# Kernel optimization log

Measured on AMD Instinct MI355X. Metric: run time of the kernel, lower is better.

Reference implementation:

```python
import jax, jax.numpy as jnp
import numpy as np

B, W, H = 8, 1024, 1024
NUM_LABELS = 100  # mask ids in [0, NUM_LABELS); 0 = background
EPS = 1e-7


def setup_inputs() -> dict:
    key = jax.random.key(0)
    k1, k2 = jax.random.split(key)
    pred = jax.random.normal(k1, (B, 2, W, H), dtype=jnp.float32)
    mask = jax.random.randint(k2, (B, W, H), 0, NUM_LABELS, dtype=jnp.int32)
    ignored_map = jnp.ones((B, W, H), dtype=jnp.float32)
    return {"pred": pred, "mask": mask, "ignored_map": ignored_map}


def _smooth_l1(d):
    # SmoothL1Loss(reduction='none'), beta=1
    a = jnp.abs(d)
    return jnp.where(a < 1.0, 0.5 * d * d, a - 0.5)


def _gt_single(mask2d):
    # Vectorized replacement of the per-instance python loop:
    # segment-mean for centroids, segment-max for the per-instance `norm`.
    seg = mask2d.reshape(-1)  # [W*H]
    x_map = jnp.tile(jnp.arange(H, dtype=jnp.float32), W)    # column index (x)
    y_map = jnp.repeat(jnp.arange(W, dtype=jnp.float32), H)  # row index (y)
    cnt = jax.ops.segment_sum(jnp.ones_like(x_map), seg, num_segments=NUM_LABELS)
    safe_cnt = jnp.maximum(cnt, 1.0)
    xc = (jax.ops.segment_sum(x_map, seg, num_segments=NUM_LABELS) / safe_cnt)[seg]
    yc = (jax.ops.segment_sum(y_map, seg, num_segments=NUM_LABELS) / safe_cnt)[seg]
    fg = (seg != 0).astype(jnp.float32)  # label 0 is background (index_list[1:])
    vx = (x_map - xc) * fg  # (x_map - mean_x) * nuclei, instances are disjoint
    vy = (y_map - yc) * fg
    # torch.max over the whole image of (coord - c)*nuclei == max(seg_max, 0)
    mx = jnp.maximum(jax.ops.segment_max(vx, seg, num_segments=NUM_LABELS), 0.0)
    my = jnp.maximum(jax.ops.segment_max(vy, seg, num_segments=NUM_LABELS), 0.0)
    gx = vx / jnp.where(mx == 0.0, 1.0, mx)[seg]  # norm(): divide by max iff max != 0
    gy = vy / jnp.where(my == 0.0, 1.0, my)[seg]
    return jnp.stack([gx, gy]).reshape(2, W, H)


def reference(pred, mask, ignored_map):
    gt = jax.vmap(_gt_single)(mask)  # [B, 2, W, H]
    fg = (mask != 0).astype(jnp.float32)[:, None]  # [B, 1, W, H]
    bg = 1.0 - fg
    n = float(mask.size)
    # ((mask != 0) + 1e-07).sum() == fg_count + eps * numel
    fg_den = jnp.sum(fg) + EPS * n
    bg_den = jnp.sum(bg) + EPS * n
    d = _smooth_l1(pred - gt)
    ig = ignored_map[:, None]
    offset_loss = jnp.sum(d * ig * (fg / fg_den + bg / bg_den))
    return offset_loss, gt
```

## Files before the change

kernel.cpp:

```cpp
#include <hip/hip_runtime.h>

#define NL 100
#define BB 8
#define HH 1024
#define NPIX (1024 * 1024)
#define EPSF 1e-7f
#define NBLK 128
#define LBK 64
#define NLOSS (LBK * BB)

typedef float f4 __attribute__((ext_vector_type(4)));

#define OFF_ACC  0
#define OFF_TKT  1
#define OFF_M8   8
#define OFF_PART (OFF_M8 + BB * (NPIX / 4))
#define WS_NEED  ((size_t)(OFF_PART + 5 * BB * NL * NBLK) * 4)

__device__ __forceinline__ int pidx(int v, int b, int l) {
    return ((v * BB + b) * NL + l) * NBLK;
}

__global__ __launch_bounds__(256) void k_stats(const int* __restrict__ mask,
                                               unsigned* __restrict__ wsu) {
    __shared__ unsigned s_cs[4][2][NL];
    __shared__ unsigned s_mx[4][NL];
    __shared__ unsigned g_cnt[NL], g_sx[NL], g_sy[NL], g_mx[NL], g_my[NL];
    unsigned* part = wsu + OFF_PART;
    unsigned* m8   = wsu + OFF_M8;
    const int b    = blockIdx.y;
    const int blk  = blockIdx.x;
    const int wv   = threadIdx.x >> 6;
    const int lane = threadIdx.x & 63;
    if (blk == 0 && b == 0 && threadIdx.x == 0) {
        ((float*)wsu)[OFF_ACC] = 0.0f;
        wsu[OFF_TKT] = 0u;
    }
    for (int i = threadIdx.x; i < NL; i += 256) {
        g_cnt[i] = 0u; g_sx[i] = 0u; g_sy[i] = 0u; g_mx[i] = 0u; g_my[i] = 0u;
    }
    for (int i = lane; i < 2 * NL; i += 64) s_cs[wv][0][i] = 0u;
    for (int i = lane; i < NL; i += 64) s_mx[wv][i] = 0u;
    __syncthreads();

    const int4* m4  = (const int4*)(mask + (size_t)b * NPIX);
    unsigned*   m8b = m8 + (size_t)b * (NPIX / 4);
    const int y0 = blk * 8 + wv * 2;

    int4 R[2][4];
#pragma unroll
    for (int r = 0; r < 2; ++r)
#pragma unroll
        for (int it = 0; it < 4; ++it)
            R[r][it] = m4[(y0 + r) * 256 + it * 64 + lane];

#pragma unroll
    for (int r = 0; r < 2; ++r) {
        unsigned* tp = &s_cs[wv][r][0];
        unsigned* mp = &s_mx[wv][0];
        const int y = y0 + r;
#pragma unroll
        for (int it = 0; it < 4; ++it) {
            const int4 mv = R[r][it];
            const int c4 = it * 64 + lane;
            const unsigned v0 = (1u << 21) + (unsigned)(c4 << 2);
            atomicAdd(tp + mv.x, v0);      atomicMax(mp + mv.x, v0);
            atomicAdd(tp + mv.y, v0 + 1u); atomicMax(mp + mv.y, v0 + 1u);
            atomicAdd(tp + mv.z, v0 + 2u); atomicMax(mp + mv.z, v0 + 2u);
            atomicAdd(tp + mv.w, v0 + 3u); atomicMax(mp + mv.w, v0 + 3u);
            m8b[y * 256 + c4] = (unsigned)mv.x | ((unsigned)mv.y << 8) |
                                ((unsigned)mv.z << 16) | ((unsigned)mv.w << 24);
        }
    }
    for (int e = lane; e < NL; e += 64) {
        const unsigned cs0 = s_cs[wv][0][e];
        const unsigned cs1 = s_cs[wv][1][e];
        const unsigned c0 = cs0 >> 21, c1 = cs1 >> 21;
        const unsigned cnt = c0 + c1;
        if (cnt) {
            atomicAdd(&g_cnt[e], cnt);
            atomicAdd(&g_sx[e], (cs0 & 0x1FFFFFu) + (cs1 & 0x1FFFFFu));
            atomicAdd(&g_sy[e], c0 * (unsigned)y0 + c1 * (unsigned)(y0 + 1));
            atomicMax(&g_my[e], c1 ? (unsigned)(y0 + 1) : (unsigned)y0);
            atomicMax(&g_mx[e], s_mx[wv][e] & 0x1FFFFFu);
        }
    }
    __syncthreads();
    for (int e = threadIdx.x; e < NL; e += 256) {
        part[pidx(0, b, e) + blk] = g_cnt[e];
        part[pidx(1, b, e) + blk] = g_sx[e];
        part[pidx(2, b, e) + blk] = g_sy[e];
        part[pidx(3, b, e) + blk] = g_mx[e];
        part[pidx(4, b, e) + blk] = g_my[e];
    }
}

__global__ __launch_bounds__(256, 2) void k_loss(const float* __restrict__ pred,
                                                 const float* __restrict__ ig,
                                                 unsigned* __restrict__ wsu,
                                                 float* __restrict__ out) {
    __shared__ unsigned s_st[5][NL];
    __shared__ unsigned s_c0[BB];
    __shared__ f4 s_tab[NL];
    __shared__ float s_red[4];
    const unsigned* part = wsu + OFF_PART;
    const unsigned* m8   = wsu + OFF_M8;
    const int b   = blockIdx.y;
    const int tid = threadIdx.x;

    if (tid < BB) s_c0[tid] = 0u;
    __syncthreads();
    {
        const int bb = tid >> 5, j = tid & 31;
        const uint4* p4 = (const uint4*)(part + pidx(0, bb, 0));
        const uint4 u = p4[j];
        atomicAdd(&s_c0[bb], u.x + u.y + u.z + u.w);
    }
    for (int t = tid; t < 5 * NL; t += 256) {
        const int v = t / NL;
        const int l = t - v * NL;
        const uint4* p4 = (const uint4*)(part + pidx(v, b, l));
        unsigned s = 0u, m = 0u;
#pragma unroll 8
        for (int k = 0; k < NBLK / 4; ++k) {
            const uint4 u = p4[k];
            s += u.x + u.y + u.z + u.w;
            m = max(max(m, u.x), max(u.y, max(u.z, u.w)));
        }
        s_st[v][l] = (v >= 3) ? m : s;
    }
    __syncthreads();
    if (tid < NL) {
        const unsigned cnt = s_st[0][tid];
        const float sc = (float)(cnt ? cnt : 1u);
        const float xc = (float)s_st[1][tid] / sc;
        const float yc = (float)s_st[2][tid] / sc;
        float fmx = (float)s_st[3][tid] - xc; if (fmx < 0.0f) fmx = 0.0f;
        float fmy = (float)s_st[4][tid] - yc; if (fmy < 0.0f) fmy = 0.0f;
        f4 e;
        e.x = xc;
        e.y = yc;
        e.z = (fmx == 0.0f) ? 1.0f : 1.0f / fmx;
        e.w = (fmy == 0.0f) ? 1.0f : 1.0f / fmy;
        s_tab[tid] = e;
    }
    __syncthreads();
    float bgc = 0.0f;
#pragma unroll
    for (int i = 0; i < BB; ++i) bgc += (float)s_c0[i];
    const float n = (float)BB * (float)NPIX;
    const float inv_bg = 1.0f / (bgc + EPSF * n);
    const float inv_fg = 1.0f / ((n - bgc) + EPSF * n);

    const unsigned* m8b = m8 + (size_t)b * (NPIX / 4);
    const f4* ig4 = (const f4*)(ig + (size_t)b * NPIX);
    const f4* px4 = (const f4*)(pred + (size_t)(2 * b) * NPIX);
    const f4* py4 = (const f4*)(pred + (size_t)(2 * b + 1) * NPIX);
    f4* gx4 = (f4*)(out + 1 + (size_t)(2 * b) * NPIX);
    f4* gy4 = (f4*)(out + 1 + (size_t)(2 * b + 1) * NPIX);

    float acc = 0.0f;
#pragma unroll
    for (int g = 0; g < 4; ++g) {
        const int base = (blockIdx.x * 4 + g) * 1024;
        unsigned M8[4]; f4 IV[4], PX[4], PY[4];
#pragma unroll
        for (int it = 0; it < 4; ++it) {
            const int i4 = base + it * 256 + tid;
            M8[it] = m8b[i4];
            IV[it] = __builtin_nontemporal_load(&ig4[i4]);
            PX[it] = __builtin_nontemporal_load(&px4[i4]);
            PY[it] = __builtin_nontemporal_load(&py4[i4]);
        }
#pragma unroll
        for (int it = 0; it < 4; ++it) {
            const int i4 = base + it * 256 + tid;
            const int p  = i4 << 2;
            const float x0 = (float)(p & (HH - 1));
            const float y  = (float)(p >> 10);
            const float* igs = (const float*)&IV[it];
            const float* pxs = (const float*)&PX[it];
            const float* pys = (const float*)&PY[it];
            f4 gxv, gyv;
            float* gxa = (float*)&gxv;
            float* gya = (float*)&gyv;
#pragma unroll
            for (int j = 0; j < 4; ++j) {
                const int m = (int)((M8[it] >> (8 * j)) & 255u);
                const f4 t = s_tab[m];
                const float fgf = (m != 0) ? 1.0f : 0.0f;
                const float gx = (x0 + (float)j - t.x) * t.z * fgf;
                const float gy = (y - t.y) * t.w * fgf;
                const float w  = ((m != 0) ? inv_fg : inv_bg) * igs[j];
                const float dx = pxs[j] - gx;
                const float dy = pys[j] - gy;
                const float ax = fabsf(dx), ay = fabsf(dy);
                acc += ((ax < 1.0f) ? 0.5f * dx * dx : ax - 0.5f) * w
                     + ((ay < 1.0f) ? 0.5f * dy * dy : ay - 0.5f) * w;
                gxa[j] = gx;
                gya[j] = gy;
            }
            __builtin_nontemporal_store(gxv, &gx4[i4]);
            __builtin_nontemporal_store(gyv, &gy4[i4]);
        }
    }
#pragma unroll
    for (int off = 32; off > 0; off >>= 1) acc += __shfl_down(acc, off, 64);
    const int lane = tid & 63, wv = tid >> 6;
    if (lane == 0) s_red[wv] = acc;
    __syncthreads();
    if (tid == 0) {
        const float s = s_red[0] + s_red[1] + s_red[2] + s_red[3];
        atomicAdd((float*)wsu + OFF_ACC, s);
        __threadfence();
        const unsigned old = atomicAdd(wsu + OFF_TKT, 1u);
        if (old == NLOSS - 1) {
            __threadfence();
            out[0] = atomicAdd((float*)wsu + OFF_ACC, 0.0f);
        }
    }
}

extern "C" void kernel_launch(void* const* d_in, const int* in_sizes, int n_in,
                              void* d_out, int out_size, void* d_ws, size_t ws_size,
                              hipStream_t stream) {
    const float* pred = (const float*)d_in[0];
    const int*   mask = (const int*)d_in[1];
    const float* ig   = (const float*)d_in[2];
    float* out = (float*)d_out;
    unsigned* wsu = (unsigned*)d_ws;

    k_stats<<<dim3(NBLK, BB), 256, 0, stream>>>(mask, wsu);
    k_loss<<<dim3(LBK, BB), 256, 0, stream>>>(pred, ig, wsu, out);
}
```

Measured before the change: 211.5 us.

## Finalize per-label stats in last stats block; shrink loss blocks for occupancy

The per-image centroid/norm table is now built once by the last-arriving k_stats block, selected with a per-image ticket counter. Each k_loss block used to re-reduce all partials itself; now it just loads the finished table. The partial layout is transposed, and the loss grid grows to 256 blocks per image with one 1024-vector chunk each and launch bounds of 4, to raise parallelism and occupancy. A memset resets the counters before the launches, which adds a small extra operation per call.

```diff
diff --git a/kernel.cpp b/kernel.cpp
--- a/kernel.cpp
+++ b/kernel.cpp
@@ -6,19 +6,21 @@
 #define NPIX (1024 * 1024)
 #define EPSF 1e-7f
 #define NBLK 128
-#define LBK 64
-#define NLOSS (LBK * BB)
+#define LGX 256
+#define NLOSS (LGX * BB)
 
 typedef float f4 __attribute__((ext_vector_type(4)));
 
 #define OFF_ACC  0
 #define OFF_TKT  1
-#define OFF_M8   8
+#define OFF_STK  2
+#define OFF_TAB  16
+#define OFF_CNT0 (OFF_TAB + 4 * BB * NL)
+#define OFF_M8   (OFF_CNT0 + BB)
 #define OFF_PART (OFF_M8 + BB * (NPIX / 4))
-#define WS_NEED  ((size_t)(OFF_PART + 5 * BB * NL * NBLK) * 4)
-
-__device__ __forceinline__ int pidx(int v, int b, int l) {
-    return ((v * BB + b) * NL + l) * NBLK;
+
+__device__ __forceinline__ int part_idx(int v, int blk, int b, int l) {
+    return ((v * NBLK + blk) * BB + b) * NL + l;
 }
 
 __global__ __launch_bounds__(256) void k_stats(const int* __restrict__ mask,
@@ -26,16 +28,13 @@
     __shared__ unsigned s_cs[4][2][NL];
     __shared__ unsigned s_mx[4][NL];
     __shared__ unsigned g_cnt[NL], g_sx[NL], g_sy[NL], g_mx[NL], g_my[NL];
+    __shared__ int s_last;
     unsigned* part = wsu + OFF_PART;
     unsigned* m8   = wsu + OFF_M8;
     const int b    = blockIdx.y;
     const int blk  = blockIdx.x;
     const int wv   = threadIdx.x >> 6;
     const int lane = threadIdx.x & 63;
-    if (blk == 0 && b == 0 && threadIdx.x == 0) {
-        ((float*)wsu)[OFF_ACC] = 0.0f;
-        wsu[OFF_TKT] = 0u;
-    }
     for (int i = threadIdx.x; i < NL; i += 256) {
         g_cnt[i] = 0u; g_sx[i] = 0u; g_sy[i] = 0u; g_mx[i] = 0u; g_my[i] = 0u;
     }
@@ -87,63 +86,59 @@
     }
     __syncthreads();
     for (int e = threadIdx.x; e < NL; e += 256) {
-        part[pidx(0, b, e) + blk] = g_cnt[e];
-        part[pidx(1, b, e) + blk] = g_sx[e];
-        part[pidx(2, b, e) + blk] = g_sy[e];
-        part[pidx(3, b, e) + blk] = g_mx[e];
-        part[pidx(4, b, e) + blk] = g_my[e];
-    }
-}
-
-__global__ __launch_bounds__(256, 2) void k_loss(const float* __restrict__ pred,
-                                                 const float* __restrict__ ig,
-                                                 unsigned* __restrict__ wsu,
-                                                 float* __restrict__ out) {
-    __shared__ unsigned s_st[5][NL];
-    __shared__ unsigned s_c0[BB];
-    __shared__ f4 s_tab[NL];
-    __shared__ float s_red[4];
-    const unsigned* part = wsu + OFF_PART;
-    const unsigned* m8   = wsu + OFF_M8;
-    const int b   = blockIdx.y;
-    const int tid = threadIdx.x;
-
-    if (tid < BB) s_c0[tid] = 0u;
-    __syncthreads();
-    {
-        const int bb = tid >> 5, j = tid & 31;
-        const uint4* p4 = (const uint4*)(part + pidx(0, bb, 0));
-        const uint4 u = p4[j];
-        atomicAdd(&s_c0[bb], u.x + u.y + u.z + u.w);
-    }
-    for (int t = tid; t < 5 * NL; t += 256) {
-        const int v = t / NL;
-        const int l = t - v * NL;
-        const uint4* p4 = (const uint4*)(part + pidx(v, b, l));
-        unsigned s = 0u, m = 0u;
-#pragma unroll 8
-        for (int k = 0; k < NBLK / 4; ++k) {
-            const uint4 u = p4[k];
-            s += u.x + u.y + u.z + u.w;
-            m = max(max(m, u.x), max(u.y, max(u.z, u.w)));
-        }
-        s_st[v][l] = (v >= 3) ? m : s;
-    }
-    __syncthreads();
-    if (tid < NL) {
-        const unsigned cnt = s_st[0][tid];
+        part[part_idx(0, blk, b, e)] = g_cnt[e];
+        part[part_idx(1, blk, b, e)] = g_sx[e];
+        part[part_idx(2, blk, b, e)] = g_sy[e];
+        part[part_idx(3, blk, b, e)] = g_mx[e];
+        part[part_idx(4, blk, b, e)] = g_my[e];
+    }
+    __syncthreads();
+    if (threadIdx.x == 0) {
+        __threadfence();
+        const unsigned old = atomicAdd(wsu + OFF_STK + b, 1u);
+        s_last = (old == NBLK - 1) ? 1 : 0;
+    }
+    __syncthreads();
+    if (!s_last) return;
+    __threadfence();
+    if (threadIdx.x < NL) {
+        const int l = threadIdx.x;
+        unsigned cnt = 0, sx = 0, sy = 0, mx = 0, my = 0;
+#pragma unroll 4
+        for (int k = 0; k < NBLK; ++k) {
+            cnt += part[part_idx(0, k, b, l)];
+            sx  += part[part_idx(1, k, b, l)];
+            sy  += part[part_idx(2, k, b, l)];
+            mx = max(mx, part[part_idx(3, k, b, l)]);
+            my = max(my, part[part_idx(4, k, b, l)]);
+        }
         const float sc = (float)(cnt ? cnt : 1u);
-        const float xc = (float)s_st[1][tid] / sc;
-        const float yc = (float)s_st[2][tid] / sc;
-        float fmx = (float)s_st[3][tid] - xc; if (fmx < 0.0f) fmx = 0.0f;
-        float fmy = (float)s_st[4][tid] - yc; if (fmy < 0.0f) fmy = 0.0f;
+        const float xc = (float)sx / sc;
+        const float yc = (float)sy / sc;
+        float fmx = (float)mx - xc; if (fmx < 0.0f) fmx = 0.0f;
+        float fmy = (float)my - yc; if (fmy < 0.0f) fmy = 0.0f;
         f4 e;
         e.x = xc;
         e.y = yc;
         e.z = (fmx == 0.0f) ? 1.0f : 1.0f / fmx;
         e.w = (fmy == 0.0f) ? 1.0f : 1.0f / fmy;
-        s_tab[tid] = e;
-    }
+        ((f4*)(wsu + OFF_TAB))[b * NL + l] = e;
+        if (l == 0) wsu[OFF_CNT0 + b] = cnt;
+    }
+}
+
+__global__ __launch_bounds__(256, 4) void k_loss(const float* __restrict__ pred,
+                                                 const float* __restrict__ ig,
+                                                 unsigned* __restrict__ wsu,
+                                                 float* __restrict__ out) {
+    __shared__ f4 s_tab[NL];
+    __shared__ unsigned s_c0[BB];
+    __shared__ float s_part[4];
+    const unsigned* m8 = wsu + OFF_M8;
+    const int b = blockIdx.y;
+    for (int i = threadIdx.x; i < NL; i += 256)
+        s_tab[i] = ((const f4*)(wsu + OFF_TAB))[b * NL + i];
+    if (threadIdx.x < BB) s_c0[threadIdx.x] = wsu[OFF_CNT0 + threadIdx.x];
     __syncthreads();
     float bgc = 0.0f;
 #pragma unroll
@@ -159,58 +154,56 @@
     f4* gx4 = (f4*)(out + 1 + (size_t)(2 * b) * NPIX);
     f4* gy4 = (f4*)(out + 1 + (size_t)(2 * b + 1) * NPIX);
 
+    const int base = blockIdx.x * 1024;
+    unsigned M8[4]; f4 IV[4], PX[4], PY[4];
+#pragma unroll
+    for (int it = 0; it < 4; ++it) {
+        const int i4 = base + it * 256 + threadIdx.x;
+        M8[it] = m8b[i4];
+        IV[it] = __builtin_nontemporal_load(&ig4[i4]);
+        PX[it] = __builtin_nontemporal_load(&px4[i4]);
+        PY[it] = __builtin_nontemporal_load(&py4[i4]);
+    }
+
     float acc = 0.0f;
 #pragma unroll
-    for (int g = 0; g < 4; ++g) {
-        const int base = (blockIdx.x * 4 + g) * 1024;
-        unsigned M8[4]; f4 IV[4], PX[4], PY[4];
-#pragma unroll
-        for (int it = 0; it < 4; ++it) {
-            const int i4 = base + it * 256 + tid;
-            M8[it] = m8b[i4];
-            IV[it] = __builtin_nontemporal_load(&ig4[i4]);
-            PX[it] = __builtin_nontemporal_load(&px4[i4]);
-            PY[it] = __builtin_nontemporal_load(&py4[i4]);
-        }
-#pragma unroll
-        for (int it = 0; it < 4; ++it) {
-            const int i4 = base + it * 256 + tid;
-            const int p  = i4 << 2;
-            const float x0 = (float)(p & (HH - 1));
-            const float y  = (float)(p >> 10);
-            const float* igs = (const float*)&IV[it];
-            const float* pxs = (const float*)&PX[it];
-            const float* pys = (const float*)&PY[it];
-            f4 gxv, gyv;
-            float* gxa = (float*)&gxv;
-            float* gya = (float*)&gyv;
-#pragma unroll
-            for (int j = 0; j < 4; ++j) {
-                const int m = (int)((M8[it] >> (8 * j)) & 255u);
-                const f4 t = s_tab[m];
-                const float fgf = (m != 0) ? 1.0f : 0.0f;
-                const float gx = (x0 + (float)j - t.x) * t.z * fgf;
-                const float gy = (y - t.y) * t.w * fgf;
-                const float w  = ((m != 0) ? inv_fg : inv_bg) * igs[j];
-                const float dx = pxs[j] - gx;
-                const float dy = pys[j] - gy;
-                const float ax = fabsf(dx), ay = fabsf(dy);
-                acc += ((ax < 1.0f) ? 0.5f * dx * dx : ax - 0.5f) * w
-                     + ((ay < 1.0f) ? 0.5f * dy * dy : ay - 0.5f) * w;
-                gxa[j] = gx;
-                gya[j] = gy;
-            }
-            __builtin_nontemporal_store(gxv, &gx4[i4]);
-            __builtin_nontemporal_store(gyv, &gy4[i4]);
-        }
+    for (int it = 0; it < 4; ++it) {
+        const int i4 = base + it * 256 + threadIdx.x;
+        const int p  = i4 << 2;
+        const float x0 = (float)(p & (HH - 1));
+        const float y  = (float)(p >> 10);
+        const float* igs = (const float*)&IV[it];
+        const float* pxs = (const float*)&PX[it];
+        const float* pys = (const float*)&PY[it];
+        f4 gxv, gyv;
+        float* gxa = (float*)&gxv;
+        float* gya = (float*)&gyv;
+#pragma unroll
+        for (int j = 0; j < 4; ++j) {
+            const int m = (int)((M8[it] >> (8 * j)) & 255u);
+            const f4 t = s_tab[m];
+            const float fgf = (m != 0) ? 1.0f : 0.0f;
+            const float gx = (x0 + (float)j - t.x) * t.z * fgf;
+            const float gy = (y - t.y) * t.w * fgf;
+            const float w  = ((m != 0) ? inv_fg : inv_bg) * igs[j];
+            const float dx = pxs[j] - gx;
+            const float dy = pys[j] - gy;
+            const float ax = fabsf(dx), ay = fabsf(dy);
+            acc += ((ax < 1.0f) ? 0.5f * dx * dx : ax - 0.5f) * w
+                 + ((ay < 1.0f) ? 0.5f * dy * dy : ay - 0.5f) * w;
+            gxa[j] = gx;
+            gya[j] = gy;
+        }
+        __builtin_nontemporal_store(gxv, &gx4[i4]);
+        __builtin_nontemporal_store(gyv, &gy4[i4]);
     }
 #pragma unroll
     for (int off = 32; off > 0; off >>= 1) acc += __shfl_down(acc, off, 64);
-    const int lane = tid & 63, wv = tid >> 6;
-    if (lane == 0) s_red[wv] = acc;
-    __syncthreads();
-    if (tid == 0) {
-        const float s = s_red[0] + s_red[1] + s_red[2] + s_red[3];
+    const int lane = threadIdx.x & 63, wv = threadIdx.x >> 6;
+    if (lane == 0) s_part[wv] = acc;
+    __syncthreads();
+    if (threadIdx.x == 0) {
+        const float s = s_part[0] + s_part[1] + s_part[2] + s_part[3];
         atomicAdd((float*)wsu + OFF_ACC, s);
         __threadfence();
         const unsigned old = atomicAdd(wsu + OFF_TKT, 1u);
@@ -230,6 +223,7 @@
     float* out = (float*)d_out;
     unsigned* wsu = (unsigned*)d_ws;
 
+    (void)hipMemsetAsync(d_ws, 0, 64, stream);
     k_stats<<<dim3(NBLK, BB), 256, 0, stream>>>(mask, wsu);
-    k_loss<<<dim3(LBK, BB), 256, 0, stream>>>(pred, ig, wsu, out);
-}
+    k_loss<<<dim3(LGX, BB), 256, 0, stream>>>(pred, ig, wsu, out);
+}
```

Measured after the change: 322.7 us. 1.53x slower.

## Add partial-reduction kernel and split loss kernel into more smaller blocks

Applied to the files above, without the earlier changes.

Adds an intermediate kernel that reduces the per-block statistics into four chunks per batch. The statistics layout is transposed so these reads coalesce. The loss kernel now only combines four pre-reduced values instead of re-reading 128 partials in every block. The loss grid grows from 64 to 256 blocks per batch, each handling one tile instead of looping over four, and occupancy hints are raised. This costs an extra kernel launch and more atomics on the global accumulator, and it drops the thread fences, relying instead on an asm dependency for ordering.

```diff
diff --git a/kernel.cpp b/kernel.cpp
--- a/kernel.cpp
+++ b/kernel.cpp
@@ -6,19 +6,19 @@
 #define NPIX (1024 * 1024)
 #define EPSF 1e-7f
 #define NBLK 128
-#define LBK 64
-#define NLOSS (LBK * BB)
+#define NCH 4
+#define LGX 256
+#define NLOSS (LGX * BB)
 
 typedef float f4 __attribute__((ext_vector_type(4)));
 
 #define OFF_ACC  0
 #define OFF_TKT  1
-#define OFF_M8   8
+#define OFF_M8   16
 #define OFF_PART (OFF_M8 + BB * (NPIX / 4))
-#define WS_NEED  ((size_t)(OFF_PART + 5 * BB * NL * NBLK) * 4)
-
-__device__ __forceinline__ int pidx(int v, int b, int l) {
-    return ((v * BB + b) * NL + l) * NBLK;
+
+__device__ __forceinline__ int part_idx(int v, int blk, int b, int l) {
+    return ((v * NBLK + blk) * BB + b) * NL + l;
 }
 
 __global__ __launch_bounds__(256) void k_stats(const int* __restrict__ mask,
@@ -33,7 +33,7 @@
     const int wv   = threadIdx.x >> 6;
     const int lane = threadIdx.x & 63;
     if (blk == 0 && b == 0 && threadIdx.x == 0) {
-        ((float*)wsu)[OFF_ACC] = 0.0f;
+        wsu[OFF_ACC] = 0u;
         wsu[OFF_TKT] = 0u;
     }
     for (int i = threadIdx.x; i < NL; i += 256) {
@@ -87,47 +87,55 @@
     }
     __syncthreads();
     for (int e = threadIdx.x; e < NL; e += 256) {
-        part[pidx(0, b, e) + blk] = g_cnt[e];
-        part[pidx(1, b, e) + blk] = g_sx[e];
-        part[pidx(2, b, e) + blk] = g_sy[e];
-        part[pidx(3, b, e) + blk] = g_mx[e];
-        part[pidx(4, b, e) + blk] = g_my[e];
-    }
-}
-
-__global__ __launch_bounds__(256, 2) void k_loss(const float* __restrict__ pred,
+        part[part_idx(0, blk, b, e)] = g_cnt[e];
+        part[part_idx(1, blk, b, e)] = g_sx[e];
+        part[part_idx(2, blk, b, e)] = g_sy[e];
+        part[part_idx(3, blk, b, e)] = g_mx[e];
+        part[part_idx(4, blk, b, e)] = g_my[e];
+    }
+}
+
+__global__ __launch_bounds__(512) void k_final2(unsigned* __restrict__ wsu) {
+    unsigned* part = wsu + OFF_PART;
+    const int c = blockIdx.x, b = blockIdx.y;
+    const int t = threadIdx.x;
+    const int v = t / NL;
+    const int l = t - v * NL;
+    unsigned s = 0u, m = 0u;
+    if (t < 5 * NL) {
+#pragma unroll 4
+        for (int k = c * 32; k < c * 32 + 32; ++k) {
+            const unsigned u = part[part_idx(v, k, b, l)];
+            s += u; m = max(m, u);
+        }
+    }
+    __syncthreads();
+    if (t < 5 * NL)
+        part[part_idx(v, c * 32, b, l)] = (v >= 3) ? m : s;
+}
+
+__global__ __launch_bounds__(256, 4) void k_loss(const float* __restrict__ pred,
                                                  const float* __restrict__ ig,
                                                  unsigned* __restrict__ wsu,
                                                  float* __restrict__ out) {
     __shared__ unsigned s_st[5][NL];
-    __shared__ unsigned s_c0[BB];
     __shared__ f4 s_tab[NL];
-    __shared__ float s_red[4];
+    __shared__ unsigned s_bgc;
+    __shared__ float s_part[4];
     const unsigned* part = wsu + OFF_PART;
     const unsigned* m8   = wsu + OFF_M8;
-    const int b   = blockIdx.y;
+    const int b = blockIdx.y;
     const int tid = threadIdx.x;
 
-    if (tid < BB) s_c0[tid] = 0u;
-    __syncthreads();
-    {
-        const int bb = tid >> 5, j = tid & 31;
-        const uint4* p4 = (const uint4*)(part + pidx(0, bb, 0));
-        const uint4 u = p4[j];
-        atomicAdd(&s_c0[bb], u.x + u.y + u.z + u.w);
-    }
+    if (tid == 0) s_bgc = 0u;
     for (int t = tid; t < 5 * NL; t += 256) {
         const int v = t / NL;
         const int l = t - v * NL;
-        const uint4* p4 = (const uint4*)(part + pidx(v, b, l));
-        unsigned s = 0u, m = 0u;
-#pragma unroll 8
-        for (int k = 0; k < NBLK / 4; ++k) {
-            const uint4 u = p4[k];
-            s += u.x + u.y + u.z + u.w;
-            m = max(max(m, u.x), max(u.y, max(u.z, u.w)));
-        }
-        s_st[v][l] = (v >= 3) ? m : s;
+        const unsigned a0 = part[part_idx(v,  0, b, l)];
+        const unsigned a1 = part[part_idx(v, 32, b, l)];
+        const unsigned a2 = part[part_idx(v, 64, b, l)];
+        const unsigned a3 = part[part_idx(v, 96, b, l)];
+        s_st[v][l] = (v >= 3) ? max(max(a0, a1), max(a2, a3)) : (a0 + a1 + a2 + a3);
     }
     __syncthreads();
     if (tid < NL) {
@@ -144,10 +152,12 @@
         e.w = (fmy == 0.0f) ? 1.0f : 1.0f / fmy;
         s_tab[tid] = e;
     }
-    __syncthreads();
-    float bgc = 0.0f;
-#pragma unroll
-    for (int i = 0; i < BB; ++i) bgc += (float)s_c0[i];
+    if (tid < NCH * BB) {
+        const int c = tid >> 3, bb = tid & 7;
+        atomicAdd(&s_bgc, part[part_idx(0, c * 32, bb, 0)]);
+    }
+    __syncthreads();
+    const float bgc = (float)s_bgc;
     const float n = (float)BB * (float)NPIX;
     const float inv_bg = 1.0f / (bgc + EPSF * n);
     const float inv_fg = 1.0f / ((n - bgc) + EPSF * n);
@@ -159,63 +169,60 @@
     f4* gx4 = (f4*)(out + 1 + (size_t)(2 * b) * NPIX);
     f4* gy4 = (f4*)(out + 1 + (size_t)(2 * b + 1) * NPIX);
 
+    const int base = blockIdx.x * 1024;
+    unsigned M8[4]; f4 IV[4], PX[4], PY[4];
+#pragma unroll
+    for (int it = 0; it < 4; ++it) {
+        const int i4 = base + it * 256 + tid;
+        M8[it] = m8b[i4];
+        IV[it] = __builtin_nontemporal_load(&ig4[i4]);
+        PX[it] = __builtin_nontemporal_load(&px4[i4]);
+        PY[it] = __builtin_nontemporal_load(&py4[i4]);
+    }
+
     float acc = 0.0f;
 #pragma unroll
-    for (int g = 0; g < 4; ++g) {
-        const int base = (blockIdx.x * 4 + g) * 1024;
-        unsigned M8[4]; f4 IV[4], PX[4], PY[4];
-#pragma unroll
-        for (int it = 0; it < 4; ++it) {
-            const int i4 = base + it * 256 + tid;
-            M8[it] = m8b[i4];
-            IV[it] = __builtin_nontemporal_load(&ig4[i4]);
-            PX[it] = __builtin_nontemporal_load(&px4[i4]);
-            PY[it] = __builtin_nontemporal_load(&py4[i4]);
-        }
-#pragma unroll
-        for (int it = 0; it < 4; ++it) {
-            const int i4 = base + it * 256 + tid;
-            const int p  = i4 << 2;
-            const float x0 = (float)(p & (HH - 1));
-            const float y  = (float)(p >> 10);
-            const float* igs = (const float*)&IV[it];
-            const float* pxs = (const float*)&PX[it];
-            const float* pys = (const float*)&PY[it];
-            f4 gxv, gyv;
-            float* gxa = (float*)&gxv;
-            float* gya = (float*)&gyv;
-#pragma unroll
-            for (int j = 0; j < 4; ++j) {
-                const int m = (int)((M8[it] >> (8 * j)) & 255u);
-                const f4 t = s_tab[m];
-                const float fgf = (m != 0) ? 1.0f : 0.0f;
-                const float gx = (x0 + (float)j - t.x) * t.z * fgf;
-                const float gy = (y - t.y) * t.w * fgf;
-                const float w  = ((m != 0) ? inv_fg : inv_bg) * igs[j];
-                const float dx = pxs[j] - gx;
-                const float dy = pys[j] - gy;
-                const float ax = fabsf(dx), ay = fabsf(dy);
-                acc += ((ax < 1.0f) ? 0.5f * dx * dx : ax - 0.5f) * w
-                     + ((ay < 1.0f) ? 0.5f * dy * dy : ay - 0.5f) * w;
-                gxa[j] = gx;
-                gya[j] = gy;
-            }
-            __builtin_nontemporal_store(gxv, &gx4[i4]);
-            __builtin_nontemporal_store(gyv, &gy4[i4]);
-        }
+    for (int it = 0; it < 4; ++it) {
+        const int i4 = base + it * 256 + tid;
+        const int p  = i4 << 2;
+        const float x0 = (float)(p & (HH - 1));
+        const float y  = (float)(p >> 10);
+        const float* igs = (const float*)&IV[it];
+        const float* pxs = (const float*)&PX[it];
+        const float* pys = (const float*)&PY[it];
+        f4 gxv, gyv;
+        float* gxa = (float*)&gxv;
+        float* gya = (float*)&gyv;
+#pragma unroll
+        for (int j = 0; j < 4; ++j) {
+            const int m = (int)((M8[it] >> (8 * j)) & 255u);
+            const f4 t = s_tab[m];
+            const float fgf = (m != 0) ? 1.0f : 0.0f;
+            const float gx = (x0 + (float)j - t.x) * t.z * fgf;
+            const float gy = (y - t.y) * t.w * fgf;
+            const float w  = ((m != 0) ? inv_fg : inv_bg) * igs[j];
+            const float dx = pxs[j] - gx;
+            const float dy = pys[j] - gy;
+            const float ax = fabsf(dx), ay = fabsf(dy);
+            acc += ((ax < 1.0f) ? 0.5f * dx * dx : ax - 0.5f) * w
+                 + ((ay < 1.0f) ? 0.5f * dy * dy : ay - 0.5f) * w;
+            gxa[j] = gx;
+            gya[j] = gy;
+        }
+        __builtin_nontemporal_store(gxv, &gx4[i4]);
+        __builtin_nontemporal_store(gyv, &gy4[i4]);
     }
 #pragma unroll
     for (int off = 32; off > 0; off >>= 1) acc += __shfl_down(acc, off, 64);
     const int lane = tid & 63, wv = tid >> 6;
-    if (lane == 0) s_red[wv] = acc;
+    if (lane == 0) s_part[wv] = acc;
     __syncthreads();
     if (tid == 0) {
-        const float s = s_red[0] + s_red[1] + s_red[2] + s_red[3];
-        atomicAdd((float*)wsu + OFF_ACC, s);
-        __threadfence();
-        const unsigned old = atomicAdd(wsu + OFF_TKT, 1u);
-        if (old == NLOSS - 1) {
-            __threadfence();
+        const float s = s_part[0] + s_part[1] + s_part[2] + s_part[3];
+        const float old = atomicAdd((float*)wsu + OFF_ACC, s);
+        asm volatile("" : : "v"(old) : "memory");
+        const unsigned t = atomicAdd(wsu + OFF_TKT, 1u);
+        if (t == NLOSS - 1) {
             out[0] = atomicAdd((float*)wsu + OFF_ACC, 0.0f);
         }
     }
@@ -231,5 +238,6 @@
     unsigned* wsu = (unsigned*)d_ws;
 
     k_stats<<<dim3(NBLK, BB), 256, 0, stream>>>(mask, wsu);
-    k_loss<<<dim3(LBK, BB), 256, 0, stream>>>(pred, ig, wsu, out);
-}
+    k_final2<<<dim3(NCH, BB), 512, 0, stream>>>(wsu);
+    k_loss<<<dim3(LGX, BB), 256, 0, stream>>>(pred, ig, wsu, out);
+}
```

Result: faster. 207.0 us (-2.1%).
